# Performance work log

Hardware: AMD Instinct MI355X
Metric: run time of the kernel (lower is better)

## Reference

```python
import jax, jax.numpy as jnp
import numpy as np

NUM_EVAL_NEGATIVES = 999  # rconst.NUM_EVAL_NEGATIVES
ROW = NUM_EVAL_NEGATIVES + 1  # 1000 candidates per user (1 positive + 999 negatives)
TOP_K = 10                # rconst.TOP_K
NUM_USERS = 8192


def setup_inputs() -> dict:
    key = jax.random.key(0)
    k1, k2 = jax.random.split(key)
    logits = jax.random.normal(k1, (NUM_USERS * ROW, 1, 2), dtype=jnp.float32)
    dup_mask = jax.random.randint(k2, (NUM_USERS * ROW, 1, 1), 0, 2, dtype=jnp.int32)
    return {"logits": logits, "dup_mask": dup_mask}


def reference(logits, dup_mask):
    # metric_fn: cast mask to float, slice off channel 0 of the softmax pair
    dup = dup_mask.astype(jnp.float32)
    l = logits[:, :, 1:]

    # compute_top_k_and_ndcg (match_mlperf=True)
    logits_by_user = l.reshape(-1, ROW)            # [U, 1000]
    dup_by_user = dup.reshape(-1, ROW)             # [U, 1000]

    # mask duplicate candidates to dtype min
    big_neg = jnp.finfo(logits_by_user.dtype).min
    logits_by_user = logits_by_user * (1.0 - dup_by_user) + dup_by_user * big_neg

    # descending argsort; position of the true item (index 0) in the ranking
    sort_indices = jnp.argsort(-logits_by_user, axis=1)  # [U, 1000]
    ranks = jnp.arange(ROW, dtype=logits_by_user.dtype)  # [1000]
    position_vector = jnp.sum(
        (sort_indices == 0).astype(logits_by_user.dtype) * ranks, axis=1)  # [U]

    in_top_k = (position_vector < TOP_K).astype(jnp.float32)
    ndcg = jnp.log(2.0) / jnp.log(position_vector + 2.0) * in_top_k

    # padded rows: all negatives are duplicates
    metric_weights = (jnp.sum(dup_by_user, axis=1) != NUM_EVAL_NEGATIVES).astype(jnp.float32)

    return in_top_k, ndcg, metric_weights
```

## Files before the change

### kernel.cpp

```cpp
#include <hip/hip_runtime.h>
#include <hip/hip_bf16.h>
#include <float.h>

#define ROW 1000
#define TOP_K 10
#define NUM_EVAL_NEG 999

__global__ __launch_bounds__(256) void metric_kernel(
    const float* __restrict__ logits,
    const int*   __restrict__ dup,
    float* __restrict__ out,
    int num_users)
{
    const int user = blockIdx.x;
    if (user >= num_users) return;
    const long long base = (long long)user * ROW;
    const float BIG_NEG = -FLT_MAX;

    const int   d0 = dup[base];
    const float l0 = logits[2 * base + 1];
    const float x0 = d0 ? BIG_NEG : l0;

    const int tid = threadIdx.x;
    const float2* lg2 = reinterpret_cast<const float2*>(logits) + base;
    const int* dp = dup + base;

    int cnt = 0;
    int dsum = 0;

    for (int j = tid; j < ROW; j += 256) {
        float2 lp = lg2[j];
        int d = dp[j];
        float m = d ? BIG_NEG : lp.y;
        cnt  += (m > x0) ? 1 : 0;
        dsum += d;
    }

    #pragma unroll
    for (int off = 32; off > 0; off >>= 1) {
        cnt  += __shfl_down(cnt, off, 64);
        dsum += __shfl_down(dsum, off, 64);
    }

    __shared__ int s_cnt[4], s_dsum[4];
    const int wave = tid >> 6;
    if ((tid & 63) == 0) { s_cnt[wave] = cnt; s_dsum[wave] = dsum; }
    __syncthreads();

    if (tid == 0) {
        int c  = s_cnt[0] + s_cnt[1] + s_cnt[2] + s_cnt[3];
        int ds = s_dsum[0] + s_dsum[1] + s_dsum[2] + s_dsum[3];
        float pos  = (float)c;
        float itk  = (pos < (float)TOP_K) ? 1.0f : 0.0f;
        float ndcg = (itk != 0.0f) ? (0.69314718055994530942f / logf(pos + 2.0f)) : 0.0f;
        float w    = (ds != NUM_EVAL_NEG) ? 1.0f : 0.0f;
        out[user]                 = itk;
        out[num_users + user]     = ndcg;
        out[2 * num_users + user] = w;
    }
}

extern "C" void kernel_launch(void* const* d_in, const int* in_sizes, int n_in,
                              void* d_out, int out_size, void* d_ws, size_t ws_size,
                              hipStream_t stream) {
    const float* logits = (const float*)d_in[0];
    const int*   dup    = (const int*)d_in[1];
    float* out = (float*)d_out;

    const int num_users = in_sizes[0] / (2 * ROW);

    metric_kernel<<<num_users, 256, 0, stream>>>(logits, dup, out, num_users);
}
```

Measured before the change: 112.1 us.

## Map one wavefront per user and vectorize loads with float4/int2

Each 256-thread block now processes four users, one per 64-lane wavefront, so the reduction finishes with wave shuffles alone and the shared-memory stage and block barrier are gone. Loads are widened to float4 for logit pairs and int2 for the duplicate mask, so each lane handles two candidates per iteration. This cuts per-user synchronization and instruction overhead and gives each lane more independent work. It depends on 16-byte alignment of each user's logit row, which holds for a row length of 1000.

```diff
diff --git a/kernel.cpp b/kernel.cpp
--- a/kernel.cpp
+++ b/kernel.cpp
@@ -3,8 +3,10 @@
 #include <float.h>
 
 #define ROW 1000
+#define ROW4 (ROW / 2)
 #define TOP_K 10
 #define NUM_EVAL_NEG 999
+#define USERS_PER_BLOCK 4
 
 __global__ __launch_bounds__(256) void metric_kernel(
     const float* __restrict__ logits,
@@ -12,28 +14,33 @@
     float* __restrict__ out,
     int num_users)
 {
-    const int user = blockIdx.x;
+    const int tid  = threadIdx.x;
+    const int lane = tid & 63;
+    const int user = blockIdx.x * USERS_PER_BLOCK + (tid >> 6);
     if (user >= num_users) return;
+
+    const float BIG_NEG = -FLT_MAX;
     const long long base = (long long)user * ROW;
-    const float BIG_NEG = -FLT_MAX;
 
     const int   d0 = dup[base];
     const float l0 = logits[2 * base + 1];
     const float x0 = d0 ? BIG_NEG : l0;
 
-    const int tid = threadIdx.x;
-    const float2* lg2 = reinterpret_cast<const float2*>(logits) + base;
-    const int* dp = dup + base;
+    const float4* lg4 = reinterpret_cast<const float4*>(logits + 2 * base);
+    const int2*   dp2 = reinterpret_cast<const int2*>(dup + base);
 
     int cnt = 0;
     int dsum = 0;
 
-    for (int j = tid; j < ROW; j += 256) {
-        float2 lp = lg2[j];
-        int d = dp[j];
-        float m = d ? BIG_NEG : lp.y;
-        cnt  += (m > x0) ? 1 : 0;
-        dsum += d;
+    #pragma unroll 2
+    for (int j = lane; j < ROW4; j += 64) {
+        float4 lp = lg4[j];
+        int2   d  = dp2[j];
+        float m0 = d.x ? BIG_NEG : lp.y;
+        float m1 = d.y ? BIG_NEG : lp.w;
+        cnt  += (m0 > x0) ? 1 : 0;
+        cnt  += (m1 > x0) ? 1 : 0;
+        dsum += d.x + d.y;
     }
 
     #pragma unroll
@@ -42,18 +49,11 @@
         dsum += __shfl_down(dsum, off, 64);
     }
 
-    __shared__ int s_cnt[4], s_dsum[4];
-    const int wave = tid >> 6;
-    if ((tid & 63) == 0) { s_cnt[wave] = cnt; s_dsum[wave] = dsum; }
-    __syncthreads();
-
-    if (tid == 0) {
-        int c  = s_cnt[0] + s_cnt[1] + s_cnt[2] + s_cnt[3];
-        int ds = s_dsum[0] + s_dsum[1] + s_dsum[2] + s_dsum[3];
-        float pos  = (float)c;
+    if (lane == 0) {
+        float pos  = (float)cnt;
         float itk  = (pos < (float)TOP_K) ? 1.0f : 0.0f;
         float ndcg = (itk != 0.0f) ? (0.69314718055994530942f / logf(pos + 2.0f)) : 0.0f;
-        float w    = (ds != NUM_EVAL_NEG) ? 1.0f : 0.0f;
+        float w    = (dsum != NUM_EVAL_NEG) ? 1.0f : 0.0f;
         out[user]                 = itk;
         out[num_users + user]     = ndcg;
         out[2 * num_users + user] = w;
@@ -68,6 +68,7 @@
     float* out = (float*)d_out;
 
     const int num_users = in_sizes[0] / (2 * ROW);
+    const int grid = (num_users + USERS_PER_BLOCK - 1) / USERS_PER_BLOCK;
 
-    metric_kernel<<<num_users, 256, 0, stream>>>(logits, dup, out, num_users);
+    metric_kernel<<<grid, 256, 0, stream>>>(logits, dup, out, num_users);
 }
```

New measurement: 111.1 us. About the same (-0.9%).
